# Optimization experiments

Measured on AMD Instinct MI355X. Metric: run time of the kernel, lower is better.

## Reference

```python
import jax, jax.numpy as jnp
import numpy as np

N, E, H, C = 50000, 1_600_000, 4, 32
DIN, DE = 128, 32
NEG_SLOPE = 0.2  # PyG GATConv leaky_relu negative_slope default


def setup_inputs() -> dict:
    key = jax.random.key(0)
    ks = jax.random.split(key, 12)
    s = 0.1  # weight scale
    return {
        "x": jax.random.normal(ks[0], (N, DIN), jnp.float32),
        "edge_index": jax.random.randint(ks[1], (2, E), 0, N, jnp.int32),
        "edge_attr": jax.random.normal(ks[2], (E, DE), jnp.float32),
        "W": jax.random.normal(ks[3], (DIN, H * C), jnp.float32) * s,
        "att_src": jax.random.normal(ks[4], (H, C), jnp.float32) * s,
        "att_dst": jax.random.normal(ks[5], (H, C), jnp.float32) * s,
        "lin_edge_W": jax.random.normal(ks[6], (DE, H * C), jnp.float32) * s,
        "att_edge": jax.random.normal(ks[7], (H, C), jnp.float32) * s,
        "bias": jax.random.normal(ks[8], (H * C,), jnp.float32) * s,
        "proj_W": jax.random.normal(ks[9], (H * C, C), jnp.float32) * s,
        "proj_b": jax.random.normal(ks[10], (C,), jnp.float32) * s,
    }


def reference(x, edge_index, edge_attr, W, att_src, att_dst, lin_edge_W,
              att_edge, bias, proj_W, proj_b):
    n = x.shape[0]
    h, c = att_src.shape
    src, dst = edge_index[0], edge_index[1]

    # add self loops; loop edge_attr = mean of incoming edge_attr (PyG fill_value='mean')
    deg = jax.ops.segment_sum(jnp.ones(src.shape, x.dtype), dst, num_segments=n)
    ea_mean = jax.ops.segment_sum(edge_attr, dst, num_segments=n) / jnp.maximum(deg, 1.0)[:, None]
    loop = jnp.arange(n, dtype=src.dtype)
    src = jnp.concatenate([src, loop])
    dst = jnp.concatenate([dst, loop])
    ea = jnp.concatenate([edge_attr, ea_mean], axis=0)

    xl = (x @ W).reshape(n, h, c)                       # [N,H,C]
    a_src = jnp.einsum('nhc,hc->nh', xl, att_src)       # [N,H]
    a_dst = jnp.einsum('nhc,hc->nh', xl, att_dst)
    e = (ea @ lin_edge_W).reshape(-1, h, c)             # [E',H,C]
    a_e = jnp.einsum('ehc,hc->eh', e, att_edge)

    alpha = jax.nn.leaky_relu(a_src[src] + a_dst[dst] + a_e, NEG_SLOPE)  # [E',H]
    amax = jax.lax.stop_gradient(jax.ops.segment_max(alpha, dst, num_segments=n))
    alpha = jnp.exp(alpha - amax[dst])
    denom = jax.ops.segment_sum(alpha, dst, num_segments=n)
    alpha = alpha / (denom[dst] + 1e-16)                # segment softmax over incoming edges

    out = jax.ops.segment_sum(xl[src] * alpha[..., None], dst, num_segments=n)  # [N,H,C]
    out = out.reshape(n, h * c) + bias                  # concat heads + bias
    return out @ proj_W + proj_b                        # concat projection
```

## Files before the change

kernel.cpp:

```cpp
#include <hip/hip_runtime.h>

#define NEG_SLOPE 0.2f

__device__ __forceinline__ float lrelu(float x) { return x > 0.0f ? x : NEG_SLOPE * x; }

__device__ __forceinline__ float bcast(float v, int srcLane) {
  return __int_as_float(__builtin_amdgcn_readlane(__float_as_int(v), srcLane));
}

__device__ __forceinline__ unsigned pack_bf16(float a, float b) {
  unsigned ua = __float_as_uint(a), ub = __float_as_uint(b);
  ua += 0x7fffu + ((ua >> 16) & 1u);
  ub += 0x7fffu + ((ub >> 16) & 1u);
  return (ua >> 16) | (ub & 0xffff0000u);
}
__device__ __forceinline__ float bf16lo(unsigned z) { return __uint_as_float(z << 16); }
__device__ __forceinline__ float bf16hi(unsigned z) { return __uint_as_float(z & 0xffff0000u); }

__global__ void k0_setup(const float* __restrict__ W, const float* __restrict__ proj_W,
                         const float* __restrict__ att_src, const float* __restrict__ att_dst,
                         const float* __restrict__ lin_edge_W, const float* __restrict__ att_edge,
                         const float* __restrict__ bias, const float* __restrict__ proj_b,
                         float* __restrict__ Wz, float* __restrict__ Ws, float* __restrict__ Wd,
                         float* __restrict__ M, float* __restrict__ cproj) {
  int t = blockIdx.x * blockDim.x + threadIdx.x;
  if (t < 16384) {
    int d = t >> 7, o = t & 127;
    int h = o >> 5, jj = o & 31;
    float s = 0.f;
    #pragma unroll
    for (int c = 0; c < 32; ++c)
      s += W[d * 128 + h * 32 + c] * proj_W[(h * 32 + c) * 32 + jj];
    Wz[d * 128 + o] = s;
  } else if (t < 16384 + 512) {
    int idx = t - 16384; int d = idx >> 2, h = idx & 3;
    float s = 0.f;
    #pragma unroll
    for (int c = 0; c < 32; ++c) s += W[d * 128 + h * 32 + c] * att_src[h * 32 + c];
    Ws[d * 4 + h] = s;
  } else if (t < 16384 + 1024) {
    int idx = t - 16384 - 512; int d = idx >> 2, h = idx & 3;
    float s = 0.f;
    #pragma unroll
    for (int c = 0; c < 32; ++c) s += W[d * 128 + h * 32 + c] * att_dst[h * 32 + c];
    Wd[d * 4 + h] = s;
  } else if (t < 16384 + 1024 + 128) {
    int idx = t - 16384 - 1024; int d = idx >> 2, h = idx & 3;
    float s = 0.f;
    #pragma unroll
    for (int c = 0; c < 32; ++c) s += lin_edge_W[d * 128 + h * 32 + c] * att_edge[h * 32 + c];
    M[d * 4 + h] = s;
  } else if (t < 16384 + 1024 + 128 + 32) {
    int jj = t - 16384 - 1024 - 128;
    float s = proj_b[jj];
    #pragma unroll
    for (int k = 0; k < 128; ++k) s += bias[k] * proj_W[k * 32 + jj];
    cproj[jj] = s;
  }
}

__global__ __launch_bounds__(256) void k1_edge(
    const int* __restrict__ dst, int E, const float4* __restrict__ ea4,
    const float* __restrict__ Mg,
    float4* __restrict__ ae_out, int* __restrict__ deg, int* __restrict__ rank) {
  __shared__ float4 s_ea[256 * 9];
  __shared__ float4 Msh[32];
  int t = threadIdx.x;
  if (t < 32) Msh[t] = ((const float4*)Mg)[t];
  int B0 = blockIdx.x * 256;
  #pragma unroll
  for (int k = 0; k < 8; ++k) {
    int f = k * 256 + t;
    int e = B0 + (f >> 3);
    float4 v = (e < E) ? ea4[(size_t)B0 * 8 + f] : make_float4(0.f, 0.f, 0.f, 0.f);
    s_ea[(f >> 3) * 9 + (f & 7)] = v;
  }
  __syncthreads();
  int e = B0 + t;
  if (e >= E) return;
  float ae0 = 0.f, ae1 = 0.f, ae2 = 0.f, ae3 = 0.f;
  #pragma unroll
  for (int j = 0; j < 8; ++j) {
    float4 v = s_ea[t * 9 + j];
    float4 m0 = Msh[j * 4 + 0], m1 = Msh[j * 4 + 1], m2 = Msh[j * 4 + 2], m3 = Msh[j * 4 + 3];
    ae0 += v.x * m0.x + v.y * m1.x + v.z * m2.x + v.w * m3.x;
    ae1 += v.x * m0.y + v.y * m1.y + v.z * m2.y + v.w * m3.y;
    ae2 += v.x * m0.z + v.y * m1.z + v.z * m2.z + v.w * m3.z;
    ae3 += v.x * m0.w + v.y * m1.w + v.z * m2.w + v.w * m3.w;
  }
  ae_out[e] = make_float4(ae0, ae1, ae2, ae3);
  rank[e] = atomicAdd(&deg[dst[e]], 1);
}

__global__ void k2_scan(const int* __restrict__ deg, int n, int* __restrict__ offsets) {
  __shared__ int shw[16];
  __shared__ int shtot;
  int tid = threadIdx.x;
  int lane = tid & 63, wid = tid >> 6;
  int running = 0;
  for (int base = 0; base < n; base += 4096) {
    int i = base + tid * 4;
    int4 v = make_int4(0, 0, 0, 0);
    if (i + 3 < n) v = *(const int4*)&deg[i];
    else {
      if (i < n) v.x = deg[i];
      if (i + 1 < n) v.y = deg[i + 1];
      if (i + 2 < n) v.z = deg[i + 2];
      if (i + 3 < n) v.w = deg[i + 3];
    }
    int tsum = v.x + v.y + v.z + v.w;
    int inc = tsum;
    #pragma unroll
    for (int s = 1; s < 64; s <<= 1) {
      int t = __shfl_up(inc, s);
      if (lane >= s) inc += t;
    }
    if (lane == 63) shw[wid] = inc;
    __syncthreads();
    if (wid == 0) {
      int w = (lane < 16) ? shw[lane] : 0;
      int winc = w;
      #pragma unroll
      for (int s = 1; s < 16; s <<= 1) {
        int t = __shfl_up(winc, s);
        if (lane >= s) winc += t;
      }
      if (lane < 16) shw[lane] = winc - w;
      if (lane == 15) shtot = winc;
    }
    __syncthreads();
    int excl = running + shw[wid] + inc - tsum;
    if (i < n)     offsets[i + 1] = excl + v.x;
    if (i + 1 < n) offsets[i + 2] = excl + v.x + v.y;
    if (i + 2 < n) offsets[i + 3] = excl + v.x + v.y + v.z;
    if (i + 3 < n) offsets[i + 4] = excl + tsum;
    running += shtot;
    __syncthreads();
  }
  if (tid == 0) offsets[0] = 0;
}

__global__ __launch_bounds__(256) void k3_gemm(
    const float* __restrict__ x, const float* __restrict__ Wz,
    const float* __restrict__ Ws, const float* __restrict__ Wd,
    int n, unsigned* __restrict__ Zp, float* __restrict__ a_src, float* __restrict__ a_dst) {
  __shared__ float2 Wl[128 * 64];
  int tid = threadIdx.x;
  for (int idx = tid; idx < 128 * 64; idx += 256) {
    int k = idx >> 6, l = idx & 63;
    Wl[idx] = make_float2(Wz[k * 128 + l], Wz[k * 128 + 64 + l]);
  }
  __syncthreads();
  int lane = tid & 63, wid = tid >> 6;
  float ws0[4], ws1[4], wd0[4], wd1[4];
  #pragma unroll
  for (int h = 0; h < 4; ++h) {
    ws0[h] = Ws[lane * 4 + h];  ws1[h] = Ws[(64 + lane) * 4 + h];
    wd0[h] = Wd[lane * 4 + h];  wd1[h] = Wd[(64 + lane) * 4 + h];
  }
  int gw = blockIdx.x * 4 + wid;
  int nw = gridDim.x * 4;
  for (int base = gw * 4; base < n; base += nw * 4) {
    float xa[4], xb[4];
    #pragma unroll
    for (int u = 0; u < 4; ++u) {
      int node = base + u;
      xa[u] = (node < n) ? x[node * 128 + lane] : 0.0f;
      xb[u] = (node < n) ? x[node * 128 + 64 + lane] : 0.0f;
    }
    float acc0[4] = {0.f, 0.f, 0.f, 0.f}, acc1[4] = {0.f, 0.f, 0.f, 0.f};
    #pragma unroll 16
    for (int k = 0; k < 64; ++k) {
      float2 w = Wl[k * 64 + lane];
      #pragma unroll
      for (int u = 0; u < 4; ++u) {
        float xv = bcast(xa[u], k);
        acc0[u] += xv * w.x; acc1[u] += xv * w.y;
      }
    }
    #pragma unroll 16
    for (int k = 0; k < 64; ++k) {
      float2 w = Wl[(64 + k) * 64 + lane];
      #pragma unroll
      for (int u = 0; u < 4; ++u) {
        float xv = bcast(xb[u], k);
        acc0[u] += xv * w.x; acc1[u] += xv * w.y;
      }
    }
    #pragma unroll
    for (int u = 0; u < 4; ++u) {
      int node = base + u;
      if (node >= n) break;
      Zp[(size_t)node * 64 + lane] = pack_bf16(acc0[u], acc1[u]);
      float ps[4], pd[4];
      #pragma unroll
      for (int h = 0; h < 4; ++h) {
        ps[h] = xa[u] * ws0[h] + xb[u] * ws1[h];
        pd[h] = xa[u] * wd0[h] + xb[u] * wd1[h];
      }
      #pragma unroll
      for (int m = 1; m < 64; m <<= 1) {
        #pragma unroll
        for (int h = 0; h < 4; ++h) {
          ps[h] += __shfl_xor(ps[h], m);
          pd[h] += __shfl_xor(pd[h], m);
        }
      }
      if (lane == 0) {
        *(float4*)&a_src[node * 4] = make_float4(ps[0], ps[1], ps[2], ps[3]);
        *(float4*)&a_dst[node * 4] = make_float4(pd[0], pd[1], pd[2], pd[3]);
      }
    }
  }
}

__global__ void k4_perm(const int* __restrict__ dst, int E,
                        const int* __restrict__ rank, const int* __restrict__ offsets,
                        int* __restrict__ perm) {
  int e = blockIdx.x * blockDim.x + threadIdx.x;
  if (e < E) perm[offsets[dst[e]] + rank[e]] = e;
}

__global__ __launch_bounds__(256) void k5_agg(
    const int* __restrict__ offsets, const int* __restrict__ perm,
    const int* __restrict__ ei_src, const float4* __restrict__ ae4,
    const unsigned* __restrict__ Zp,
    const float* __restrict__ a_src, const float* __restrict__ a_dst,
    const float* __restrict__ cproj, int n, float* __restrict__ out) {
  __shared__ float4 s_w[4][64];
  __shared__ int    s_s[4][64];
  int tid = threadIdx.x;
  int lane = tid & 63, wid = tid >> 6;
  int gw = blockIdx.x * 4 + wid, nw = gridDim.x * 4;
  int h0 = lane >> 5, j = lane & 31;
  float cp = cproj[j];
  const float* wbase = (const float*)&s_w[wid][0];
  for (int node = gw; node < n; node += nw) {
    int off0 = offsets[node], off1 = offsets[node + 1];
    int dg = off1 - off0;
    float4 ad = *(const float4*)&a_dst[node * 4];
    float dsx = 0.f, dsy = 0.f, dsz = 0.f, dsw = 0.f;
    float aex = 0.f, aey = 0.f, aez = 0.f, aew = 0.f;
    float agg0 = 0.f, agg1 = 0.f;
    for (int base = off0; base < off1; base += 64) {
      int rem = off1 - base; if (rem > 64) rem = 64;
      int i = base + lane;
      if (lane < rem) {
        int e = perm[i];
        int s = ei_src[e];
        float4 a = ae4[e];
        float4 as = *(const float4*)&a_src[s * 4];
        float4 w;
        w.x = __expf(lrelu(a.x + as.x + ad.x));
        w.y = __expf(lrelu(a.y + as.y + ad.y));
        w.z = __expf(lrelu(a.z + as.z + ad.z));
        w.w = __expf(lrelu(a.w + as.w + ad.w));
        dsx += w.x; dsy += w.y; dsz += w.z; dsw += w.w;
        aex += a.x; aey += a.y; aez += a.z; aew += a.w;
        s_w[wid][lane] = make_float4(w.x, w.z, w.y, w.w);
        s_s[wid][lane] = s;
      }
      int jj = 0;
      for (; jj + 4 <= rem; jj += 4) {
        int s0 = s_s[wid][jj], s1 = s_s[wid][jj + 1];
        int s2 = s_s[wid][jj + 2], s3 = s_s[wid][jj + 3];
        unsigned z0 = Zp[(size_t)s0 * 64 + lane];
        unsigned z1 = Zp[(size_t)s1 * 64 + lane];
        unsigned z2 = Zp[(size_t)s2 * 64 + lane];
        unsigned z3 = Zp[(size_t)s3 * 64 + lane];
        float2 w0 = *(const float2*)(wbase + (jj    ) * 4 + 2 * h0);
        float2 w1 = *(const float2*)(wbase + (jj + 1) * 4 + 2 * h0);
        float2 w2 = *(const float2*)(wbase + (jj + 2) * 4 + 2 * h0);
        float2 w3 = *(const float2*)(wbase + (jj + 3) * 4 + 2 * h0);
        agg0 += w0.x * bf16lo(z0) + w1.x * bf16lo(z1) + w2.x * bf16lo(z2) + w3.x * bf16lo(z3);
        agg1 += w0.y * bf16hi(z0) + w1.y * bf16hi(z1) + w2.y * bf16hi(z2) + w3.y * bf16hi(z3);
      }
      for (; jj < rem; ++jj) {
        int s0 = s_s[wid][jj];
        unsigned z0 = Zp[(size_t)s0 * 64 + lane];
        float2 w0 = *(const float2*)(wbase + jj * 4 + 2 * h0);
        agg0 += w0.x * bf16lo(z0);
        agg1 += w0.y * bf16hi(z0);
      }
    }
    #pragma unroll
    for (int m = 1; m < 64; m <<= 1) {
      dsx += __shfl_xor(dsx, m); dsy += __shfl_xor(dsy, m);
      dsz += __shfl_xor(dsz, m); dsw += __shfl_xor(dsw, m);
      aex += __shfl_xor(aex, m); aey += __shfl_xor(aey, m);
      aez += __shfl_xor(aez, m); aew += __shfl_xor(aew, m);
    }
    float invd = 1.0f / (float)(dg > 0 ? dg : 1);
    float4 asn = *(const float4*)&a_src[node * 4];
    float w0 = __expf(lrelu(asn.x + ad.x + aex * invd));
    float w1 = __expf(lrelu(asn.y + ad.y + aey * invd));
    float w2 = __expf(lrelu(asn.z + ad.z + aez * invd));
    float w3 = __expf(lrelu(asn.w + ad.w + aew * invd));
    dsx += w0; dsy += w1; dsz += w2; dsw += w3;
    unsigned zpn = Zp[(size_t)node * 64 + lane];
    float sw0 = h0 ? w1 : w0, sw1 = h0 ? w3 : w2;
    agg0 += sw0 * bf16lo(zpn);
    agg1 += sw1 * bf16hi(zpn);
    float d0 = h0 ? dsy : dsx, d1 = h0 ? dsw : dsz;
    float tt = agg0 / (d0 + 1e-16f) + agg1 / (d1 + 1e-16f);
    tt += __shfl_xor(tt, 32);
    if (lane < 32) out[node * 32 + j] = tt + cp;
  }
}

extern "C" void kernel_launch(void* const* d_in, const int* in_sizes, int n_in,
                              void* d_out, int out_size, void* d_ws, size_t ws_size,
                              hipStream_t stream) {
  const float* x          = (const float*)d_in[0];
  const int*   ei         = (const int*)  d_in[1];
  const float* ea         = (const float*)d_in[2];
  const float* W          = (const float*)d_in[3];
  const float* att_src    = (const float*)d_in[4];
  const float* att_dst    = (const float*)d_in[5];
  const float* lin_edge_W = (const float*)d_in[6];
  const float* att_edge   = (const float*)d_in[7];
  const float* bias       = (const float*)d_in[8];
  const float* proj_W     = (const float*)d_in[9];
  const float* proj_b     = (const float*)d_in[10];
  float* out = (float*)d_out;
  int N = in_sizes[0] / 128;
  int E = in_sizes[1] / 2;

  char* p = (char*)d_ws;
  auto alloc = [&](size_t bytes) {
    char* r = p;
    p += (bytes + 255) & ~(size_t)255;
    return r;
  };
  unsigned* Zp     = (unsigned*)alloc((size_t)N * 64 * 4);
  float* a_src     = (float*)alloc((size_t)N * 4 * 4);
  float* a_dst     = (float*)alloc((size_t)N * 4 * 4);
  int*   deg       = (int*)  alloc((size_t)N * 4);
  int*   offsets   = (int*)  alloc((size_t)(N + 1) * 4);
  int*   rank      = (int*)  alloc((size_t)E * 4);
  int*   perm      = (int*)  alloc((size_t)E * 4);
  float* ae_seq    = (float*)alloc((size_t)E * 16);
  float* Wz        = (float*)alloc(128 * 128 * 4);
  float* Ws        = (float*)alloc(128 * 4 * 4);
  float* Wd        = (float*)alloc(128 * 4 * 4);
  float* M         = (float*)alloc(32 * 4 * 4);
  float* cproj     = (float*)alloc(32 * 4);

  hipMemsetAsync(deg, 0, (size_t)N * 4, stream);

  k0_setup<<<69, 256, 0, stream>>>(W, proj_W, att_src, att_dst, lin_edge_W, att_edge,
                                   bias, proj_b, Wz, Ws, Wd, M, cproj);
  k1_edge<<<(E + 255) / 256, 256, 0, stream>>>(ei + E, E, (const float4*)ea, M,
                                               (float4*)ae_seq, deg, rank);
  k2_scan<<<1, 1024, 0, stream>>>(deg, N, offsets);
  k3_gemm<<<512, 256, 0, stream>>>(x, Wz, Ws, Wd, N, Zp, a_src, a_dst);
  k4_perm<<<(E + 255) / 256, 256, 0, stream>>>(ei + E, E, rank, offsets, perm);
  k5_agg<<<2048, 256, 0, stream>>>(offsets, perm, ei, (const float4*)ae_seq, Zp,
                                   a_src, a_dst, cproj, N, out);
}
```

Baseline: 570.8 us.

## Precompute edge softmax weights in edge pass and scatter packed CSR records

The node GEMM now runs before the edge kernel, so the edge kernel can gather a_src/a_dst and compute the exp'd attention logits per edge. These are packed as bf16 together with the edge attention term. A scatter kernel writes each edge's source index and packed weights into a dst-sorted CSR array. The aggregation kernel then reads sequential records instead of chasing perm -> src -> ae -> a_src indirections. This trades random gathers in the aggregation for an extra 32-byte-per-edge scatter and bf16 rounding of the weights and edge terms.

```diff
diff --git a/kernel.cpp b/kernel.cpp
--- a/kernel.cpp
+++ b/kernel.cpp
@@ -59,10 +59,85 @@
   }
 }
 
+__global__ __launch_bounds__(256) void k3_gemm(
+    const float* __restrict__ x, const float* __restrict__ Wz,
+    const float* __restrict__ Ws, const float* __restrict__ Wd,
+    int n, unsigned* __restrict__ Zp, float* __restrict__ a_src, float* __restrict__ a_dst) {
+  __shared__ float2 Wl[128 * 64];
+  int tid = threadIdx.x;
+  for (int idx = tid; idx < 128 * 64; idx += 256) {
+    int k = idx >> 6, l = idx & 63;
+    Wl[idx] = make_float2(Wz[k * 128 + l], Wz[k * 128 + 64 + l]);
+  }
+  __syncthreads();
+  int lane = tid & 63, wid = tid >> 6;
+  float ws0[4], ws1[4], wd0[4], wd1[4];
+  #pragma unroll
+  for (int h = 0; h < 4; ++h) {
+    ws0[h] = Ws[lane * 4 + h];  ws1[h] = Ws[(64 + lane) * 4 + h];
+    wd0[h] = Wd[lane * 4 + h];  wd1[h] = Wd[(64 + lane) * 4 + h];
+  }
+  int gw = blockIdx.x * 4 + wid;
+  int nw = gridDim.x * 4;
+  for (int base = gw * 4; base < n; base += nw * 4) {
+    float xa[4], xb[4];
+    #pragma unroll
+    for (int u = 0; u < 4; ++u) {
+      int node = base + u;
+      xa[u] = (node < n) ? x[node * 128 + lane] : 0.0f;
+      xb[u] = (node < n) ? x[node * 128 + 64 + lane] : 0.0f;
+    }
+    float acc0[4] = {0.f, 0.f, 0.f, 0.f}, acc1[4] = {0.f, 0.f, 0.f, 0.f};
+    #pragma unroll 16
+    for (int k = 0; k < 64; ++k) {
+      float2 w = Wl[k * 64 + lane];
+      #pragma unroll
+      for (int u = 0; u < 4; ++u) {
+        float xv = bcast(xa[u], k);
+        acc0[u] += xv * w.x; acc1[u] += xv * w.y;
+      }
+    }
+    #pragma unroll 16
+    for (int k = 0; k < 64; ++k) {
+      float2 w = Wl[(64 + k) * 64 + lane];
+      #pragma unroll
+      for (int u = 0; u < 4; ++u) {
+        float xv = bcast(xb[u], k);
+        acc0[u] += xv * w.x; acc1[u] += xv * w.y;
+      }
+    }
+    #pragma unroll
+    for (int u = 0; u < 4; ++u) {
+      int node = base + u;
+      if (node >= n) break;
+      Zp[(size_t)node * 64 + lane] = pack_bf16(acc0[u], acc1[u]);
+      float ps[4], pd[4];
+      #pragma unroll
+      for (int h = 0; h < 4; ++h) {
+        ps[h] = xa[u] * ws0[h] + xb[u] * ws1[h];
+        pd[h] = xa[u] * wd0[h] + xb[u] * wd1[h];
+      }
+      #pragma unroll
+      for (int m = 1; m < 64; m <<= 1) {
+        #pragma unroll
+        for (int h = 0; h < 4; ++h) {
+          ps[h] += __shfl_xor(ps[h], m);
+          pd[h] += __shfl_xor(pd[h], m);
+        }
+      }
+      if (lane == 0) {
+        *(float4*)&a_src[node * 4] = make_float4(ps[0], ps[1], ps[2], ps[3]);
+        *(float4*)&a_dst[node * 4] = make_float4(pd[0], pd[1], pd[2], pd[3]);
+      }
+    }
+  }
+}
+
 __global__ __launch_bounds__(256) void k1_edge(
-    const int* __restrict__ dst, int E, const float4* __restrict__ ea4,
+    const int* __restrict__ ei, int E, const float4* __restrict__ ea4,
     const float* __restrict__ Mg,
-    float4* __restrict__ ae_out, int* __restrict__ deg, int* __restrict__ rank) {
+    const float* __restrict__ a_src, const float* __restrict__ a_dst,
+    uint4* __restrict__ we, int* __restrict__ deg, int* __restrict__ rank) {
   __shared__ float4 s_ea[256 * 9];
   __shared__ float4 Msh[32];
   int t = threadIdx.x;
@@ -78,6 +153,9 @@
   __syncthreads();
   int e = B0 + t;
   if (e >= E) return;
+  int s = ei[e], d = ei[E + e];
+  float4 as = *(const float4*)&a_src[(size_t)s * 4];
+  float4 ad = *(const float4*)&a_dst[(size_t)d * 4];
   float ae0 = 0.f, ae1 = 0.f, ae2 = 0.f, ae3 = 0.f;
   #pragma unroll
   for (int j = 0; j < 8; ++j) {
@@ -88,8 +166,13 @@
     ae2 += v.x * m0.z + v.y * m1.z + v.z * m2.z + v.w * m3.z;
     ae3 += v.x * m0.w + v.y * m1.w + v.z * m2.w + v.w * m3.w;
   }
-  ae_out[e] = make_float4(ae0, ae1, ae2, ae3);
-  rank[e] = atomicAdd(&deg[dst[e]], 1);
+  float w0 = __expf(lrelu(ae0 + as.x + ad.x));
+  float w1 = __expf(lrelu(ae1 + as.y + ad.y));
+  float w2 = __expf(lrelu(ae2 + as.z + ad.z));
+  float w3 = __expf(lrelu(ae3 + as.w + ad.w));
+  we[e] = make_uint4(pack_bf16(w0, w1), pack_bf16(w2, w3),
+                     pack_bf16(ae0, ae1), pack_bf16(ae2, ae3));
+  rank[e] = atomicAdd(&deg[d], 1);
 }
 
 __global__ void k2_scan(const int* __restrict__ deg, int n, int* __restrict__ offsets) {
@@ -140,90 +223,21 @@
   if (tid == 0) offsets[0] = 0;
 }
 
-__global__ __launch_bounds__(256) void k3_gemm(
-    const float* __restrict__ x, const float* __restrict__ Wz,
-    const float* __restrict__ Ws, const float* __restrict__ Wd,
-    int n, unsigned* __restrict__ Zp, float* __restrict__ a_src, float* __restrict__ a_dst) {
-  __shared__ float2 Wl[128 * 64];
-  int tid = threadIdx.x;
-  for (int idx = tid; idx < 128 * 64; idx += 256) {
-    int k = idx >> 6, l = idx & 63;
-    Wl[idx] = make_float2(Wz[k * 128 + l], Wz[k * 128 + 64 + l]);
-  }
-  __syncthreads();
-  int lane = tid & 63, wid = tid >> 6;
-  float ws0[4], ws1[4], wd0[4], wd1[4];
-  #pragma unroll
-  for (int h = 0; h < 4; ++h) {
-    ws0[h] = Ws[lane * 4 + h];  ws1[h] = Ws[(64 + lane) * 4 + h];
-    wd0[h] = Wd[lane * 4 + h];  wd1[h] = Wd[(64 + lane) * 4 + h];
-  }
-  int gw = blockIdx.x * 4 + wid;
-  int nw = gridDim.x * 4;
-  for (int base = gw * 4; base < n; base += nw * 4) {
-    float xa[4], xb[4];
-    #pragma unroll
-    for (int u = 0; u < 4; ++u) {
-      int node = base + u;
-      xa[u] = (node < n) ? x[node * 128 + lane] : 0.0f;
-      xb[u] = (node < n) ? x[node * 128 + 64 + lane] : 0.0f;
-    }
-    float acc0[4] = {0.f, 0.f, 0.f, 0.f}, acc1[4] = {0.f, 0.f, 0.f, 0.f};
-    #pragma unroll 16
-    for (int k = 0; k < 64; ++k) {
-      float2 w = Wl[k * 64 + lane];
-      #pragma unroll
-      for (int u = 0; u < 4; ++u) {
-        float xv = bcast(xa[u], k);
-        acc0[u] += xv * w.x; acc1[u] += xv * w.y;
-      }
-    }
-    #pragma unroll 16
-    for (int k = 0; k < 64; ++k) {
-      float2 w = Wl[(64 + k) * 64 + lane];
-      #pragma unroll
-      for (int u = 0; u < 4; ++u) {
-        float xv = bcast(xb[u], k);
-        acc0[u] += xv * w.x; acc1[u] += xv * w.y;
-      }
-    }
-    #pragma unroll
-    for (int u = 0; u < 4; ++u) {
-      int node = base + u;
-      if (node >= n) break;
-      Zp[(size_t)node * 64 + lane] = pack_bf16(acc0[u], acc1[u]);
-      float ps[4], pd[4];
-      #pragma unroll
-      for (int h = 0; h < 4; ++h) {
-        ps[h] = xa[u] * ws0[h] + xb[u] * ws1[h];
-        pd[h] = xa[u] * wd0[h] + xb[u] * wd1[h];
-      }
-      #pragma unroll
-      for (int m = 1; m < 64; m <<= 1) {
-        #pragma unroll
-        for (int h = 0; h < 4; ++h) {
-          ps[h] += __shfl_xor(ps[h], m);
-          pd[h] += __shfl_xor(pd[h], m);
-        }
-      }
-      if (lane == 0) {
-        *(float4*)&a_src[node * 4] = make_float4(ps[0], ps[1], ps[2], ps[3]);
-        *(float4*)&a_dst[node * 4] = make_float4(pd[0], pd[1], pd[2], pd[3]);
-      }
-    }
-  }
-}
-
-__global__ void k4_perm(const int* __restrict__ dst, int E,
-                        const int* __restrict__ rank, const int* __restrict__ offsets,
-                        int* __restrict__ perm) {
+__global__ void k4_scatter(const int* __restrict__ ei, int E,
+                           const int* __restrict__ rank, const int* __restrict__ offsets,
+                           const uint4* __restrict__ we, uint4* __restrict__ csr) {
   int e = blockIdx.x * blockDim.x + threadIdx.x;
-  if (e < E) perm[offsets[dst[e]] + rank[e]] = e;
+  if (e >= E) return;
+  int s = ei[e], d = ei[E + e];
+  int slot = offsets[d] + rank[e];
+  uint4 w = we[e];
+  uint4* ent = &csr[(size_t)slot * 2];
+  *(int*)ent = s;
+  ent[1] = w;
 }
 
 __global__ __launch_bounds__(256) void k5_agg(
-    const int* __restrict__ offsets, const int* __restrict__ perm,
-    const int* __restrict__ ei_src, const float4* __restrict__ ae4,
+    const int* __restrict__ offsets, const uint4* __restrict__ csr,
     const unsigned* __restrict__ Zp,
     const float* __restrict__ a_src, const float* __restrict__ a_dst,
     const float* __restrict__ cproj, int n, float* __restrict__ out) {
@@ -238,26 +252,21 @@
   for (int node = gw; node < n; node += nw) {
     int off0 = offsets[node], off1 = offsets[node + 1];
     int dg = off1 - off0;
-    float4 ad = *(const float4*)&a_dst[node * 4];
     float dsx = 0.f, dsy = 0.f, dsz = 0.f, dsw = 0.f;
     float aex = 0.f, aey = 0.f, aez = 0.f, aew = 0.f;
     float agg0 = 0.f, agg1 = 0.f;
     for (int base = off0; base < off1; base += 64) {
       int rem = off1 - base; if (rem > 64) rem = 64;
-      int i = base + lane;
       if (lane < rem) {
-        int e = perm[i];
-        int s = ei_src[e];
-        float4 a = ae4[e];
-        float4 as = *(const float4*)&a_src[s * 4];
-        float4 w;
-        w.x = __expf(lrelu(a.x + as.x + ad.x));
-        w.y = __expf(lrelu(a.y + as.y + ad.y));
-        w.z = __expf(lrelu(a.z + as.z + ad.z));
-        w.w = __expf(lrelu(a.w + as.w + ad.w));
-        dsx += w.x; dsy += w.y; dsz += w.z; dsw += w.w;
-        aex += a.x; aey += a.y; aez += a.z; aew += a.w;
-        s_w[wid][lane] = make_float4(w.x, w.z, w.y, w.w);
+        const uint4* ent = &csr[(size_t)(base + lane) * 2];
+        int s = *(const int*)ent;
+        uint4 w = ent[1];
+        float w0 = bf16lo(w.x), w1 = bf16hi(w.x);
+        float w2 = bf16lo(w.y), w3 = bf16hi(w.y);
+        dsx += w0; dsy += w1; dsz += w2; dsw += w3;
+        aex += bf16lo(w.z); aey += bf16hi(w.z);
+        aez += bf16lo(w.w); aew += bf16hi(w.w);
+        s_w[wid][lane] = make_float4(w0, w2, w1, w3);
         s_s[wid][lane] = s;
       }
       int jj = 0;
@@ -292,6 +301,7 @@
     }
     float invd = 1.0f / (float)(dg > 0 ? dg : 1);
     float4 asn = *(const float4*)&a_src[node * 4];
+    float4 ad  = *(const float4*)&a_dst[node * 4];
     float w0 = __expf(lrelu(asn.x + ad.x + aex * invd));
     float w1 = __expf(lrelu(asn.y + ad.y + aey * invd));
     float w2 = __expf(lrelu(asn.z + ad.z + aez * invd));
@@ -338,8 +348,8 @@
   int*   deg       = (int*)  alloc((size_t)N * 4);
   int*   offsets   = (int*)  alloc((size_t)(N + 1) * 4);
   int*   rank      = (int*)  alloc((size_t)E * 4);
-  int*   perm      = (int*)  alloc((size_t)E * 4);
-  float* ae_seq    = (float*)alloc((size_t)E * 16);
+  uint4* we        = (uint4*)alloc((size_t)E * 16);
+  uint4* csr       = (uint4*)alloc((size_t)E * 32);
   float* Wz        = (float*)alloc(128 * 128 * 4);
   float* Ws        = (float*)alloc(128 * 4 * 4);
   float* Wd        = (float*)alloc(128 * 4 * 4);
@@ -350,11 +360,10 @@
 
   k0_setup<<<69, 256, 0, stream>>>(W, proj_W, att_src, att_dst, lin_edge_W, att_edge,
                                    bias, proj_b, Wz, Ws, Wd, M, cproj);
-  k1_edge<<<(E + 255) / 256, 256, 0, stream>>>(ei + E, E, (const float4*)ea, M,
-                                               (float4*)ae_seq, deg, rank);
+  k3_gemm<<<512, 256, 0, stream>>>(x, Wz, Ws, Wd, N, Zp, a_src, a_dst);
+  k1_edge<<<(E + 255) / 256, 256, 0, stream>>>(ei, E, (const float4*)ea, M,
+                                               a_src, a_dst, we, deg, rank);
   k2_scan<<<1, 1024, 0, stream>>>(deg, N, offsets);
-  k3_gemm<<<512, 256, 0, stream>>>(x, Wz, Ws, Wd, N, Zp, a_src, a_dst);
-  k4_perm<<<(E + 255) / 256, 256, 0, stream>>>(ei + E, E, rank, offsets, perm);
-  k5_agg<<<2048, 256, 0, stream>>>(offsets, perm, ei, (const float4*)ae_seq, Zp,
-                                   a_src, a_dst, cproj, N, out);
-}
+  k4_scatter<<<(E + 255) / 256, 256, 0, stream>>>(ei, E, rank, offsets, we, csr);
+  k5_agg<<<2048, 256, 0, stream>>>(offsets, csr, Zp, a_src, a_dst, cproj, N, out);
+}
```

Result: faster. 558.2 us (-2.2%).
